# Kernel tuning notes

Hardware: AMD Instinct MI355X
Metric: run time of the kernel (lower is better)

The kernel has to match this reference:

```python
import jax, jax.numpy as jnp
import numpy as np

COULOMB_CONSTANT = -1.0
EV = 1.602e-19
MAX_ELEMENT = 100
N_ATOMS = 4096
HIDDEN = 16
EMB_ROWS = MAX_ELEMENT * (MAX_ELEMENT + 1) // 2  # 5050


def setup_inputs() -> dict:
    key = jax.random.key(0)
    ks = jax.random.split(key, 8)
    coordinates = jax.random.normal(ks[0], (N_ATOMS, 3), dtype=jnp.float32) * 5.0
    atom_ix = jax.random.randint(ks[1], (N_ATOMS,), 0, MAX_ELEMENT)
    charges = jax.random.normal(ks[2], (N_ATOMS,), dtype=jnp.float32)
    # embedding table [EMB_ROWS, 1]
    emb = jax.random.normal(ks[3], (EMB_ROWS, 1), dtype=jnp.float32)
    # FeedforwardNetwork sizes [2] + [16] + [3]: Linear(2,16), ReLU, Linear(16,3)
    W1 = jax.random.normal(ks[4], (2, HIDDEN), dtype=jnp.float32) / np.sqrt(2.0)
    b1 = jnp.zeros((HIDDEN,), dtype=jnp.float32)
    W2 = jax.random.normal(ks[5], (HIDDEN, 3), dtype=jnp.float32) / np.sqrt(HIDDEN)
    b2 = jnp.zeros((3,), dtype=jnp.float32)
    bias = jax.random.normal(ks[6], (1,), dtype=jnp.float32)
    return {"coordinates": coordinates, "atom_ix": atom_ix, "charges": charges,
            "emb": emb, "W1": W1, "b1": b1, "W2": W2, "b2": b2, "bias": bias}


def reference(coordinates, atom_ix, charges, emb, W1, b1, W2, b2, bias):
    # pairwise distances [N, N]
    diff = coordinates[None, :, :] - coordinates[:, None, :]
    sq = jnp.sum(diff * diff, axis=-1)
    pos = sq > 0
    d_safe = jnp.sqrt(jnp.where(pos, sq, 1.0))
    # torch: nan_to_num(1/d, 0.0) maps diagonal inf -> huge -> clamped to 10
    reciprocal_d = jnp.where(pos, jnp.minimum(1.0 / d_safe, 10.0), 10.0)
    # pairwise embedding gather: index i*(i+1)//2 + j
    pairwise_atom_ix = atom_ix[:, None] * (atom_ix[:, None] + 1) // 2 + atom_ix[None, :]
    pairwise_atom_emb = emb[pairwise_atom_ix, 0]  # [N, N]
    pairwise_charges = charges[:, None] * charges[None, :]  # [N, N]
    model_inputs = jnp.stack([pairwise_atom_emb, pairwise_charges], axis=-1)  # [N, N, 2]
    # tiny MLP: 2 -> 16 -> 3
    h = jax.nn.relu(jnp.einsum('nmi,ih->nmh', model_inputs, W1) + b1)
    atom_weights = jnp.einsum('nmh,ho->nmo', h, W2) + b2  # [N, N, 3]
    c_weights = atom_weights[..., 0]
    lj_sigma = atom_weights[..., 1]
    lj_r = atom_weights[..., 2]
    c_energy = COULOMB_CONSTANT * jnp.sum(c_weights * reciprocal_d)
    sr = lj_sigma * reciprocal_d
    sr6 = sr ** 6
    lj_energy = EV * jnp.sum(lj_r * (sr6 * sr6 - sr6))
    return c_energy + lj_energy + bias
```

## Files before the change

### kernel.cpp

```cpp
#include <hip/hip_runtime.h>
#include <hip/hip_bf16.h>
#include <stdint.h>

#define THREADS 256
#define ROWS_PER_BLOCK 8
#define JSPLIT 2
#define EMB_ROWS 5050
#define PACK_OFF 65536

typedef _Float16 half2v __attribute__((ext_vector_type(2)));
typedef __fp16   fp16x2 __attribute__((ext_vector_type(2)));

__device__ __forceinline__ half2v pk(float a, float b) {
    fp16x2 r = __builtin_amdgcn_cvt_pkrtz(a, b);
    return __builtin_bit_cast(half2v, r);
}
__device__ __forceinline__ half2v pkfma(half2v a, half2v b, half2v c) {
    return __builtin_elementwise_fma(a, b, c);
}

__global__ __launch_bounds__(THREADS) void pack_kernel(
    const float* __restrict__ coords, const float* __restrict__ charges,
    float4* __restrict__ pack, int n)
{
    const int i = blockIdx.x * THREADS + threadIdx.x;
    if (i < n)
        pack[i] = make_float4(coords[3 * i], coords[3 * i + 1],
                              coords[3 * i + 2], charges[i]);
}

__global__ __launch_bounds__(THREADS) void energy_main_kernel(
    const float4* __restrict__ pack,
    const int*    __restrict__ atom_ix,
    const float*  __restrict__ emb,
    const float*  __restrict__ W1,
    const float*  __restrict__ b1,
    const float*  __restrict__ W2,
    const float*  __restrict__ b2,
    float* __restrict__ partials,
    int n_atoms)
{
    __shared__ uint32_t s_emb2[EMB_ROWS];
    for (int t = threadIdx.x; t < EMB_ROWS; t += THREADS) {
        const float e = emb[t];
        s_emb2[t] = __builtin_bit_cast(uint32_t, pk(e, e));
    }

    half2v A2[8], B2[8], C2[8], U0_2[8], U1_2[8], U2_2[8];
#pragma unroll
    for (int p = 0; p < 8; ++p) {
        A2[p]   = pk(W1[2 * p],      W1[2 * p + 1]);
        B2[p]   = pk(W1[16 + 2 * p], W1[16 + 2 * p + 1]);
        C2[p]   = pk(b1[2 * p],      b1[2 * p + 1]);
        U0_2[p] = pk(W2[3 * (2 * p) + 0], W2[3 * (2 * p + 1) + 0]);
        U1_2[p] = pk(W2[3 * (2 * p) + 1], W2[3 * (2 * p + 1) + 1]);
        U2_2[p] = pk(W2[3 * (2 * p) + 2], W2[3 * (2 * p + 1) + 2]);
    }
    const float bo0 = b2[0], bo1 = b2[1], bo2 = b2[2];

    const int rb   = blockIdx.x / JSPLIT;
    const int js   = blockIdx.x % JSPLIT;
    const int row0 = rb * ROWS_PER_BLOCK;
    const int jlen = n_atoms / JSPLIT;
    const int j0   = js * jlen;
    const int jend = j0 + jlen;

    float  xr[ROWS_PER_BLOCK], yr[ROWS_PER_BLOCK], zr[ROWS_PER_BLOCK];
    half2v qr2[ROWS_PER_BLOCK];
    int    brb4[ROWS_PER_BLOCK];
#pragma unroll
    for (int r = 0; r < ROWS_PER_BLOCK; ++r) {
        const int i = row0 + r;
        const float4 p = pack[i];
        xr[r] = p.x; yr[r] = p.y; zr[r] = p.z;
        qr2[r] = pk(p.w, p.w);
        const int a = atom_ix[i];
        brb4[r] = ((a * (a + 1)) >> 1) << 2;
    }
    __syncthreads();

    float cacc = 0.0f, ljacc = 0.0f;
    const half2v zero2 = (half2v)(_Float16)0.0f;
    const char* sbase = (const char*)s_emb2;

#pragma unroll 2
    for (int j = j0 + threadIdx.x; j < jend; j += THREADS) {
        const float4 pj = pack[j];
        const int    aj = atom_ix[j];
        const half2v qj2 = pk(pj.w, pj.w);
        const int    ajb = aj << 2;

#pragma unroll
        for (int r = 0; r < ROWS_PER_BLOCK; ++r) {
            const float dx = pj.x - xr[r];
            const float dy = pj.y - yr[r];
            const float dz = pj.z - zr[r];
            const float sq = fmaf(dx, dx, fmaf(dy, dy, dz * dz));
            const float rd = fminf(__builtin_amdgcn_rsqf(sq), 10.0f);

            const half2v e2 = *(const half2v*)(sbase + brb4[r] + ajb);
            const half2v c2 = qr2[r] * qj2;

            float o0 = bo0, o1 = bo1, o2 = bo2;
#pragma unroll
            for (int p = 0; p < 8; ++p) {
                half2v t = pkfma(c2, B2[p], C2[p]);
                t = pkfma(e2, A2[p], t);
                t = __builtin_elementwise_max(t, zero2);
                o0 = __builtin_amdgcn_fdot2(t, U0_2[p], o0, false);
                o1 = __builtin_amdgcn_fdot2(t, U1_2[p], o1, false);
                o2 = __builtin_amdgcn_fdot2(t, U2_2[p], o2, false);
            }

            cacc = fmaf(o0, rd, cacc);
            const float sr  = o1 * rd;
            const float sr2 = sr * sr;
            const float sr6 = sr2 * sr2 * sr2;
            ljacc = fmaf(o2, fmaf(sr6, sr6, -sr6), ljacc);
        }
    }

#pragma unroll
    for (int off = 32; off > 0; off >>= 1) {
        cacc  += __shfl_down(cacc, off, 64);
        ljacc += __shfl_down(ljacc, off, 64);
    }
    __shared__ float s_c[THREADS / 64], s_l[THREADS / 64];
    const int wave = threadIdx.x >> 6;
    const int lane = threadIdx.x & 63;
    if (lane == 0) { s_c[wave] = cacc; s_l[wave] = ljacc; }
    __syncthreads();
    if (threadIdx.x == 0) {
        float ct = 0.0f, lt = 0.0f;
#pragma unroll
        for (int w = 0; w < THREADS / 64; ++w) { ct += s_c[w]; lt += s_l[w]; }
        partials[2 * blockIdx.x + 0] = ct;
        partials[2 * blockIdx.x + 1] = lt;
    }
}

__global__ __launch_bounds__(THREADS, 1) void energy_reduce_kernel(
    const float* __restrict__ partials, int nblocks,
    const float* __restrict__ bias, float* __restrict__ out)
{
    float ct = 0.0f, lt = 0.0f;
    for (int b = threadIdx.x; b < nblocks; b += THREADS) {
        ct += partials[2 * b + 0];
        lt += partials[2 * b + 1];
    }
#pragma unroll
    for (int off = 32; off > 0; off >>= 1) {
        ct += __shfl_down(ct, off, 64);
        lt += __shfl_down(lt, off, 64);
    }
    __shared__ float s_c[THREADS / 64], s_l[THREADS / 64];
    const int wave = threadIdx.x >> 6;
    const int lane = threadIdx.x & 63;
    if (lane == 0) { s_c[wave] = ct; s_l[wave] = lt; }
    __syncthreads();
    if (threadIdx.x == 0) {
        float c = 0.0f, l = 0.0f;
#pragma unroll
        for (int w = 0; w < THREADS / 64; ++w) { c += s_c[w]; l += s_l[w]; }
        out[0] = -c + 1.602e-19f * l + bias[0];
    }
}

extern "C" void kernel_launch(void* const* d_in, const int* in_sizes, int n_in,
                              void* d_out, int out_size, void* d_ws, size_t ws_size,
                              hipStream_t stream)
{
    const float* coords  = (const float*)d_in[0];
    const int*   atom_ix = (const int*)d_in[1];
    const float* charges = (const float*)d_in[2];
    const float* emb     = (const float*)d_in[3];
    const float* W1      = (const float*)d_in[4];
    const float* b1      = (const float*)d_in[5];
    const float* W2      = (const float*)d_in[6];
    const float* b2      = (const float*)d_in[7];
    const float* bias    = (const float*)d_in[8];

    float*  out      = (float*)d_out;
    float*  partials = (float*)d_ws;
    float4* pack     = (float4*)((char*)d_ws + PACK_OFF);

    const int n       = in_sizes[1];
    const int nblocks = (n / ROWS_PER_BLOCK) * JSPLIT;

    pack_kernel<<<(n + THREADS - 1) / THREADS, THREADS, 0, stream>>>(
        coords, charges, pack, n);
    energy_main_kernel<<<nblocks, THREADS, 0, stream>>>(
        pack, atom_ix, emb, W1, b1, W2, b2, partials, n);
    energy_reduce_kernel<<<1, THREADS, 0, stream>>>(partials, nblocks, bias, out);
}
```

Baseline: 47.31 us.

## Evaluate per-pair MLP with MFMA 16x16x16 and lane permutes

Replaces the packed-half VALU evaluation of the 2-16-3 MLP with two chained MFMA f16 instructions per group of 16 pairs. Inputs are broadcast across lane groups and outputs gathered back with ds_bpermute. Each wave now also walks a contiguous slice of j instead of block-strided indices. The aim is to offload the multiply-add work to matrix cores, but it adds heavy padding (K=2 in a K=16 op), many permutes and selects per pair.

New measurement: 67.57 us. +42.8%, slower.

```diff
diff --git a/kernel.cpp b/kernel.cpp
--- a/kernel.cpp
+++ b/kernel.cpp
@@ -3,20 +3,23 @@
 #include <stdint.h>
 
 #define THREADS 256
+#define WAVES (THREADS / 64)
 #define ROWS_PER_BLOCK 8
 #define JSPLIT 2
 #define EMB_ROWS 5050
 #define PACK_OFF 65536
 
-typedef _Float16 half2v __attribute__((ext_vector_type(2)));
-typedef __fp16   fp16x2 __attribute__((ext_vector_type(2)));
-
-__device__ __forceinline__ half2v pk(float a, float b) {
-    fp16x2 r = __builtin_amdgcn_cvt_pkrtz(a, b);
-    return __builtin_bit_cast(half2v, r);
-}
-__device__ __forceinline__ half2v pkfma(half2v a, half2v b, half2v c) {
-    return __builtin_elementwise_fma(a, b, c);
+typedef __fp16 fp16x2 __attribute__((ext_vector_type(2)));
+typedef __fp16 half4  __attribute__((ext_vector_type(4)));
+typedef float  floatx4 __attribute__((ext_vector_type(4)));
+typedef unsigned int uint2v __attribute__((ext_vector_type(2)));
+
+__device__ __forceinline__ fp16x2 pkrtz(float a, float b) {
+    return __builtin_amdgcn_cvt_pkrtz(a, b);
+}
+__device__ __forceinline__ float bpermf(int idx_bytes, float v) {
+    return __builtin_bit_cast(float,
+        __builtin_amdgcn_ds_bpermute(idx_bytes, __builtin_bit_cast(int, v)));
 }
 
 __global__ __launch_bounds__(THREADS) void pack_kernel(
@@ -40,55 +43,57 @@
     float* __restrict__ partials,
     int n_atoms)
 {
-    __shared__ uint32_t s_emb2[EMB_ROWS];
-    for (int t = threadIdx.x; t < EMB_ROWS; t += THREADS) {
-        const float e = emb[t];
-        s_emb2[t] = __builtin_bit_cast(uint32_t, pk(e, e));
-    }
-
-    half2v A2[8], B2[8], C2[8], U0_2[8], U1_2[8], U2_2[8];
-#pragma unroll
-    for (int p = 0; p < 8; ++p) {
-        A2[p]   = pk(W1[2 * p],      W1[2 * p + 1]);
-        B2[p]   = pk(W1[16 + 2 * p], W1[16 + 2 * p + 1]);
-        C2[p]   = pk(b1[2 * p],      b1[2 * p + 1]);
-        U0_2[p] = pk(W2[3 * (2 * p) + 0], W2[3 * (2 * p + 1) + 0]);
-        U1_2[p] = pk(W2[3 * (2 * p) + 1], W2[3 * (2 * p + 1) + 1]);
-        U2_2[p] = pk(W2[3 * (2 * p) + 2], W2[3 * (2 * p + 1) + 2]);
-    }
-    const float bo0 = b2[0], bo1 = b2[1], bo2 = b2[2];
+    __shared__ float s_emb[EMB_ROWS];
+    for (int t = threadIdx.x; t < EMB_ROWS; t += THREADS) s_emb[t] = emb[t];
+
+    const int lane  = threadIdx.x & 63;
+    const int g     = lane >> 4;
+    const int row16 = lane & 15;
+
+    half4 A1 = (half4)(__fp16)0;
+    if (g == 0) {
+        const fp16x2 t = pkrtz(W1[row16], W1[16 + row16]);
+        A1[0] = t[0]; A1[1] = t[1];
+    }
+    half4 A2 = (half4)(__fp16)0;
+    if (row16 < 3) {
+#pragma unroll
+        for (int e = 0; e < 4; ++e)
+            A2[e] = (__fp16)W2[3 * (4 * g + e) + row16];
+    }
+    floatx4 C1;
+#pragma unroll
+    for (int q = 0; q < 4; ++q) C1[q] = b1[4 * g + q];
+    floatx4 C2 = {0.f, 0.f, 0.f, 0.f};
+    if (g == 0) { C2[0] = b2[0]; C2[1] = b2[1]; C2[2] = b2[2]; }
 
     const int rb   = blockIdx.x / JSPLIT;
     const int js   = blockIdx.x % JSPLIT;
     const int row0 = rb * ROWS_PER_BLOCK;
     const int jlen = n_atoms / JSPLIT;
-    const int j0   = js * jlen;
-    const int jend = j0 + jlen;
-
-    float  xr[ROWS_PER_BLOCK], yr[ROWS_PER_BLOCK], zr[ROWS_PER_BLOCK];
-    half2v qr2[ROWS_PER_BLOCK];
-    int    brb4[ROWS_PER_BLOCK];
+    const int wv   = threadIdx.x >> 6;
+    const int jw   = jlen / WAVES;
+    const int j0   = js * jlen + wv * jw;
+
+    float xr[ROWS_PER_BLOCK], yr[ROWS_PER_BLOCK], zr[ROWS_PER_BLOCK], qr[ROWS_PER_BLOCK];
+    int   br[ROWS_PER_BLOCK];
 #pragma unroll
     for (int r = 0; r < ROWS_PER_BLOCK; ++r) {
         const int i = row0 + r;
         const float4 p = pack[i];
-        xr[r] = p.x; yr[r] = p.y; zr[r] = p.z;
-        qr2[r] = pk(p.w, p.w);
+        xr[r] = p.x; yr[r] = p.y; zr[r] = p.z; qr[r] = p.w;
         const int a = atom_ix[i];
-        brb4[r] = ((a * (a + 1)) >> 1) << 2;
+        br[r] = (a * (a + 1)) >> 1;
     }
     __syncthreads();
 
     float cacc = 0.0f, ljacc = 0.0f;
-    const half2v zero2 = (half2v)(_Float16)0.0f;
-    const char* sbase = (const char*)s_emb2;
-
-#pragma unroll 2
-    for (int j = j0 + threadIdx.x; j < jend; j += THREADS) {
+
+#pragma unroll 1
+    for (int jr = 0; jr < jw; jr += 64) {
+        const int j = j0 + jr + lane;
         const float4 pj = pack[j];
         const int    aj = atom_ix[j];
-        const half2v qj2 = pk(pj.w, pj.w);
-        const int    ajb = aj << 2;
 
 #pragma unroll
         for (int r = 0; r < ROWS_PER_BLOCK; ++r) {
@@ -98,25 +103,40 @@
             const float sq = fmaf(dx, dx, fmaf(dy, dy, dz * dz));
             const float rd = fminf(__builtin_amdgcn_rsqf(sq), 10.0f);
 
-            const half2v e2 = *(const half2v*)(sbase + brb4[r] + ajb);
-            const half2v c2 = qr2[r] * qj2;
-
-            float o0 = bo0, o1 = bo1, o2 = bo2;
-#pragma unroll
-            for (int p = 0; p < 8; ++p) {
-                half2v t = pkfma(c2, B2[p], C2[p]);
-                t = pkfma(e2, A2[p], t);
-                t = __builtin_elementwise_max(t, zero2);
-                o0 = __builtin_amdgcn_fdot2(t, U0_2[p], o0, false);
-                o1 = __builtin_amdgcn_fdot2(t, U1_2[p], o1, false);
-                o2 = __builtin_amdgcn_fdot2(t, U2_2[p], o2, false);
+            const float e = s_emb[br[r] + aj];
+            const float c = qr[r] * pj.w;
+            const float pkec = __builtin_bit_cast(float, pkrtz(e, c));
+
+            floatx4 d2s[4];
+#pragma unroll
+            for (int s = 0; s < 4; ++s) {
+                float bs = bpermf(((s << 4) | row16) << 2, pkec);
+                const unsigned bu = (g == 0) ? __builtin_bit_cast(unsigned, bs) : 0u;
+                const half4 B1 = __builtin_bit_cast(half4, (uint2v){bu, 0u});
+                const floatx4 d1 =
+                    __builtin_amdgcn_mfma_f32_16x16x16f16(A1, B1, C1, 0, 0, 0);
+                const fp16x2 h01 = pkrtz(fmaxf(d1[0], 0.f), fmaxf(d1[1], 0.f));
+                const fp16x2 h23 = pkrtz(fmaxf(d1[2], 0.f), fmaxf(d1[3], 0.f));
+                const half4 B2 = {h01[0], h01[1], h23[0], h23[1]};
+                d2s[s] = __builtin_amdgcn_mfma_f32_16x16x16f16(A2, B2, C2, 0, 0, 0);
             }
 
-            cacc = fmaf(o0, rd, cacc);
-            const float sr  = o1 * rd;
+            float o[3];
+#pragma unroll
+            for (int m = 0; m < 3; ++m) {
+                const int idx = row16 << 2;
+                const float t0 = bpermf(idx, d2s[0][m]);
+                const float t1 = bpermf(idx, d2s[1][m]);
+                const float t2 = bpermf(idx, d2s[2][m]);
+                const float t3 = bpermf(idx, d2s[3][m]);
+                o[m] = (g == 0) ? t0 : (g == 1) ? t1 : (g == 2) ? t2 : t3;
+            }
+
+            cacc = fmaf(o[0], rd, cacc);
+            const float sr  = o[1] * rd;
             const float sr2 = sr * sr;
             const float sr6 = sr2 * sr2 * sr2;
-            ljacc = fmaf(o2, fmaf(sr6, sr6, -sr6), ljacc);
+            ljacc = fmaf(o[2], fmaf(sr6, sr6, -sr6), ljacc);
         }
     }
 
@@ -125,15 +145,13 @@
         cacc  += __shfl_down(cacc, off, 64);
         ljacc += __shfl_down(ljacc, off, 64);
     }
-    __shared__ float s_c[THREADS / 64], s_l[THREADS / 64];
-    const int wave = threadIdx.x >> 6;
-    const int lane = threadIdx.x & 63;
-    if (lane == 0) { s_c[wave] = cacc; s_l[wave] = ljacc; }
+    __shared__ float s_c[WAVES], s_l[WAVES];
+    if (lane == 0) { s_c[wv] = cacc; s_l[wv] = ljacc; }
     __syncthreads();
     if (threadIdx.x == 0) {
         float ct = 0.0f, lt = 0.0f;
 #pragma unroll
-        for (int w = 0; w < THREADS / 64; ++w) { ct += s_c[w]; lt += s_l[w]; }
+        for (int w = 0; w < WAVES; ++w) { ct += s_c[w]; lt += s_l[w]; }
         partials[2 * blockIdx.x + 0] = ct;
         partials[2 * blockIdx.x + 1] = lt;
     }
```

## Pin MLP weights in VGPRs, split columns four ways, drop outer unroll

Applied to the files above, without the earlier changes.

Empty asm constraints force the packed half2 MLP weights and output biases into VGPRs. This stops the compiler from rematerializing or keeping them in SGPRs, which packed-math and dot2 ops cannot take directly as operands. JSPLIT rises from 2 to 4, doubling the block count so more blocks can run at once. The j loop unroll drops from 2 to 1 to limit register pressure. In exchange each block redoes its shared embedding table load over half as many columns, and twice as many partial sums feed the final reduction.

After: 48.67 us. +2.9%, slower.

```diff
diff --git a/kernel.cpp b/kernel.cpp
--- a/kernel.cpp
+++ b/kernel.cpp
@@ -4,7 +4,7 @@
 
 #define THREADS 256
 #define ROWS_PER_BLOCK 8
-#define JSPLIT 2
+#define JSPLIT 4
 #define EMB_ROWS 5050
 #define PACK_OFF 65536
 
@@ -46,17 +46,20 @@
         s_emb2[t] = __builtin_bit_cast(uint32_t, pk(e, e));
     }
 
-    half2v A2[8], B2[8], C2[8], U0_2[8], U1_2[8], U2_2[8];
+    uint32_t A2[8], B2[8], C2[8], U0[8], U1[8], U2[8];
 #pragma unroll
     for (int p = 0; p < 8; ++p) {
-        A2[p]   = pk(W1[2 * p],      W1[2 * p + 1]);
-        B2[p]   = pk(W1[16 + 2 * p], W1[16 + 2 * p + 1]);
-        C2[p]   = pk(b1[2 * p],      b1[2 * p + 1]);
-        U0_2[p] = pk(W2[3 * (2 * p) + 0], W2[3 * (2 * p + 1) + 0]);
-        U1_2[p] = pk(W2[3 * (2 * p) + 1], W2[3 * (2 * p + 1) + 1]);
-        U2_2[p] = pk(W2[3 * (2 * p) + 2], W2[3 * (2 * p + 1) + 2]);
+        A2[p] = __builtin_bit_cast(uint32_t, pk(W1[2 * p],      W1[2 * p + 1]));
+        B2[p] = __builtin_bit_cast(uint32_t, pk(W1[16 + 2 * p], W1[16 + 2 * p + 1]));
+        C2[p] = __builtin_bit_cast(uint32_t, pk(b1[2 * p],      b1[2 * p + 1]));
+        U0[p] = __builtin_bit_cast(uint32_t, pk(W2[3 * (2 * p) + 0], W2[3 * (2 * p + 1) + 0]));
+        U1[p] = __builtin_bit_cast(uint32_t, pk(W2[3 * (2 * p) + 1], W2[3 * (2 * p + 1) + 1]));
+        U2[p] = __builtin_bit_cast(uint32_t, pk(W2[3 * (2 * p) + 2], W2[3 * (2 * p + 1) + 2]));
+        asm("" : "+v"(A2[p]), "+v"(B2[p]), "+v"(C2[p]),
+                 "+v"(U0[p]), "+v"(U1[p]), "+v"(U2[p]));
     }
-    const float bo0 = b2[0], bo1 = b2[1], bo2 = b2[2];
+    float bo0 = b2[0], bo1 = b2[1], bo2 = b2[2];
+    asm("" : "+v"(bo0), "+v"(bo1), "+v"(bo2));
 
     const int rb   = blockIdx.x / JSPLIT;
     const int js   = blockIdx.x % JSPLIT;
@@ -83,7 +86,7 @@
     const half2v zero2 = (half2v)(_Float16)0.0f;
     const char* sbase = (const char*)s_emb2;
 
-#pragma unroll 2
+#pragma unroll 1
     for (int j = j0 + threadIdx.x; j < jend; j += THREADS) {
         const float4 pj = pack[j];
         const int    aj = atom_ix[j];
@@ -104,12 +107,13 @@
             float o0 = bo0, o1 = bo1, o2 = bo2;
 #pragma unroll
             for (int p = 0; p < 8; ++p) {
-                half2v t = pkfma(c2, B2[p], C2[p]);
-                t = pkfma(e2, A2[p], t);
+                half2v t = pkfma(c2, __builtin_bit_cast(half2v, B2[p]),
+                                     __builtin_bit_cast(half2v, C2[p]));
+                t = pkfma(e2, __builtin_bit_cast(half2v, A2[p]), t);
                 t = __builtin_elementwise_max(t, zero2);
-                o0 = __builtin_amdgcn_fdot2(t, U0_2[p], o0, false);
-                o1 = __builtin_amdgcn_fdot2(t, U1_2[p], o1, false);
-                o2 = __builtin_amdgcn_fdot2(t, U2_2[p], o2, false);
+                o0 = __builtin_amdgcn_fdot2(t, __builtin_bit_cast(half2v, U0[p]), o0, false);
+                o1 = __builtin_amdgcn_fdot2(t, __builtin_bit_cast(half2v, U1[p]), o1, false);
+                o2 = __builtin_amdgcn_fdot2(t, __builtin_bit_cast(half2v, U2[p]), o2, false);
             }
 
             cacc = fmaf(o0, rd, cacc);
```
